# Kernel optimization log

Measured on AMD Instinct MI355X. Metric: run time of the kernel, lower is better.

The kernel has to match this reference:

```python
import jax, jax.numpy as jnp
import numpy as np

B, S, D = 16, 1024, 768          # batch, seq_len, in_features
NS, MAXW = 256, 8                # num_spans, max span width (fixed for jit)
V, C = 128, 6                    # num_vertexes, max corefs per vertex
R = 512                          # num_max_rels_per_example
REL, HID, DIS = 97, 384, 20      # relation_num, hidden_dim, dis_size
NEG = -1e30


def setup_inputs() -> dict:
    key = jax.random.key(0)
    ks = jax.random.split(key, 14)
    sentence_repr = jax.random.normal(ks[0], (B, S, D), jnp.float32)
    starts = jax.random.randint(ks[1], (B, NS), 0, S - MAXW)
    widths = jax.random.randint(ks[2], (B, NS), 0, MAXW)
    entity_span_indices = jnp.stack([starts, starts + widths], axis=-1)  # (B,NS,2), start<=end
    entity_span_indices_mask = jax.random.randint(ks[3], (B, NS), 0, 2)
    vertex_indices = jax.random.randint(ks[4], (B, V, C), 0, NS)
    vertex_indices_mask = jax.random.randint(ks[5], (B, V, C), 0, 2)
    head_tail_indices = jax.random.randint(ks[6], (B, R, 2), 0, V)
    relation_mask = jax.random.randint(ks[7], (B, R), 0, 2)
    dis_h_2_t = jax.random.randint(ks[8], (B, R), 0, 20)
    dis_t_2_h = jax.random.randint(ks[9], (B, R), 0, 20)
    dis_embed = jax.random.normal(ks[10], (20, DIS), jnp.float32) * 0.02
    dis_embed = dis_embed.at[10].set(0.0)  # padding_idx=10
    fin = D + DIS                      # final_in_features with distance
    in_proj = 2 * fin + D              # concat [head+dis, tail+dis, head*tail]
    W1 = jax.random.normal(ks[11], (in_proj, HID), jnp.float32) / np.float32(np.sqrt(in_proj))
    W2 = jax.random.normal(ks[12], (HID, REL), jnp.float32) / np.float32(np.sqrt(HID))
    b2 = jnp.zeros((REL,), jnp.float32)
    return dict(sentence_repr=sentence_repr, entity_span_indices=entity_span_indices,
                entity_span_indices_mask=entity_span_indices_mask,
                vertex_indices=vertex_indices, vertex_indices_mask=vertex_indices_mask,
                head_tail_indices=head_tail_indices, relation_mask=relation_mask,
                dis_h_2_t=dis_h_2_t, dis_t_2_h=dis_t_2_h,
                dis_embed=dis_embed, W1=W1, W2=W2, b2=b2)


def reference(sentence_repr, entity_span_indices, entity_span_indices_mask,
              vertex_indices, vertex_indices_mask, head_tail_indices,
              relation_mask, dis_h_2_t, dis_t_2_h, dis_embed, W1, W2, b2):
    Bx, Sx, Dx = sentence_repr.shape
    # --- SpanExtractor: masked max pooling over tokens in each span [start, end] ---
    starts = entity_span_indices[..., 0]
    ends = entity_span_indices[..., 1]
    pos = starts[..., None] + jnp.arange(MAXW)            # (B,NS,W)
    valid = pos <= ends[..., None]
    posc = jnp.clip(pos, 0, Sx - 1).reshape(Bx, -1)       # (B,NS*W)
    tok = jnp.take_along_axis(sentence_repr, posc[..., None], axis=1)
    tok = tok.reshape(Bx, NS, MAXW, Dx)
    span_emb = jnp.where(valid[..., None], tok, NEG).max(axis=2)   # (B,NS,D)
    # --- coref 'mean' pooling over spans per vertex (batched_index_select) ---
    vidx = vertex_indices.reshape(Bx, -1)
    ve = jnp.take_along_axis(span_emb, vidx[..., None], axis=1).reshape(Bx, V, C, Dx)
    m = vertex_indices_mask.astype(jnp.float32)
    cnt = jnp.maximum(m.sum(axis=2), 1.0)                 # num_corefs clamped >=1
    vertex_emb = (ve * m[..., None]).sum(axis=2) / cnt[..., None]  # (B,V,D)
    # --- head/tail gather ---
    hti = head_tail_indices.reshape(Bx, -1)
    ht = jnp.take_along_axis(vertex_emb, hti[..., None], axis=1).reshape(Bx, R, 2, Dx)
    head_repr = ht[:, :, 0, :]
    tail_repr = ht[:, :, 1, :]
    # (original multiplies by relation_mask and discards the result -> no-op)
    eh = dis_embed[dis_h_2_t]                              # (B,R,DIS)
    et = dis_embed[dis_t_2_h]
    feat = jnp.concatenate([head_repr, eh, tail_repr, et, head_repr * tail_repr], axis=-1)
    # TwoLayerLinear: relu(x @ W1) @ W2 + b2, bias=(False, True)
    predict_re = jax.nn.relu(feat @ W1) @ W2 + b2          # (B,R,REL)
    return predict_re
```

## Files before the change

kernel.cpp:

```cpp
#include <hip/hip_runtime.h>
#include <cstdint>
#include <cstddef>

#define B_    16
#define S_    1024
#define D_    768
#define NS_   256
#define V_    128
#define C_    6
#define R_    512
#define REL_  97
#define HID_  384
#define DIS_  20
#define K1_   2344
#define KP_   2432
#define NIT_  38
#define N2P_  128

#define BM1   128
#define BN1   128
#define SLICE_ ((size_t)8192 * HID_)

typedef unsigned short ushort_t;
typedef unsigned int   u32;
typedef short bf16x4 __attribute__((ext_vector_type(4)));
typedef short bf16x8 __attribute__((ext_vector_type(8)));
typedef float f32x4  __attribute__((ext_vector_type(4)));
typedef float f32x16 __attribute__((ext_vector_type(16)));

__device__ __forceinline__ float bf2f(short s) {
    return __uint_as_float(((unsigned int)(unsigned short)s) << 16);
}
__device__ __forceinline__ short f2bf(float x) {
    union { float f; unsigned int u; } c; c.f = x;
    unsigned int r = (c.u + 0x7fffu + ((c.u >> 16) & 1u)) >> 16;
    return (short)(unsigned short)r;
}

typedef const __attribute__((address_space(1))) u32* gas_t;
typedef __attribute__((address_space(3))) u32*       las_t;
__device__ __forceinline__ void dma16(const void* g, void* l) {
    __builtin_amdgcn_global_load_lds((gas_t)g, (las_t)l, 16, 0, 0);
}

__device__ __forceinline__ int w1_orig(int k) {
    if      (k < 768)  return k;
    else if (k < 1536) return k + 20;
    else if (k < 2304) return k + 40;
    else if (k < 2324) return 768 + (k - 2304);
    else if (k < K1_)  return 1556 + (k - 2324);
    return -1;
}

__global__ __launch_bounds__(192) void prep_kernel(
    const float* __restrict__ sr, const int* __restrict__ spans,
    const float* __restrict__ W1, const float* __restrict__ W2,
    ushort_t* __restrict__ span_emb, ushort_t* __restrict__ W1Tile,
    ushort_t* __restrict__ W2T)
{
    int blk = blockIdx.x;
    int tid = threadIdx.x;
    if (blk < 4096) {
        int bn    = blk;
        int b     = bn >> 8;
        int start = spans[2 * bn];
        int end   = spans[2 * bn + 1];
        int w     = end - start;
        const float* base = sr + ((size_t)b * S_ + start) * D_ + tid * 4;
        f32x4 m = *(const f32x4*)base;
        for (int j = 1; j <= w; ++j) {
            f32x4 x = *(const f32x4*)(base + (size_t)j * D_);
#pragma unroll
            for (int c = 0; c < 4; ++c) m[c] = fmaxf(m[c], x[c]);
        }
        bf16x4 o;
#pragma unroll
        for (int c = 0; c < 4; ++c) o[c] = f2bf(m[c]);
        *(bf16x4*)(span_emb + (size_t)bn * D_ + tid * 4) = o;
    } else if (blk < 4096 + NIT_) {
        int it = blk - 4096;
#pragma unroll
        for (int g = 0; g < 16; ++g) {
            int idx = g * 192 + tid;
            int nn  = idx & 127;
            int kg  = (idx >> 7) & 7;
            int nt  = idx >> 10;
            int n   = nt * 128 + nn;
            bf16x8 p;
#pragma unroll
            for (int j = 0; j < 8; ++j) {
                int k = it * 64 + kg * 8 + j;
                int orig = w1_orig(k);
                float v = (orig >= 0) ? W1[(size_t)orig * HID_ + n] : 0.f;
                p[j] = f2bf(v);
            }
            *(bf16x8*)(W1Tile + (((size_t)it * 3 + nt) * 8 + kg) * 1024 + nn * 8) = p;
        }
    } else {
        int bid = blk - 4096 - NIT_;
#pragma unroll
        for (int i = 0; i < 32; ++i) {
            int e = bid * 6144 + i * 192 + tid;
            int n = e / HID_;
            int k = e - n * HID_;
            float v = (n < REL_) ? W2[(size_t)k * REL_ + n] : 0.f;
            W2T[e] = (ushort_t)f2bf(v);
        }
    }
}

__global__ __launch_bounds__(192) void vertex_kernel(
    const ushort_t* __restrict__ span_emb, const int* __restrict__ vidx,
    const int* __restrict__ vmask, ushort_t* __restrict__ vembB)
{
    int bv = blockIdx.x;
    int b  = bv >> 7;
    const int* vi = vidx  + bv * C_;
    const int* vm = vmask + bv * C_;
    int   idxs[C_];
    float ms[C_];
    float cnt = 0.f;
#pragma unroll
    for (int c = 0; c < C_; ++c) {
        idxs[c] = vi[c];
        ms[c]   = (float)vm[c];
        cnt    += ms[c];
    }
    float inv = 1.f / fmaxf(cnt, 1.f);
    int col = threadIdx.x * 4;
    float s[4] = {0.f, 0.f, 0.f, 0.f};
#pragma unroll
    for (int c = 0; c < C_; ++c) {
        if (ms[c] != 0.f) {
            bf16x4 x = *(const bf16x4*)(span_emb +
                        ((size_t)(b * NS_ + idxs[c])) * D_ + col);
#pragma unroll
            for (int q = 0; q < 4; ++q) s[q] += bf2f(x[q]);
        }
    }
    bf16x4 o;
#pragma unroll
    for (int q = 0; q < 4; ++q) o[q] = f2bf(s[q] * inv);
    *(bf16x4*)(vembB + (size_t)bv * D_ + col) = o;
}

__global__ __launch_bounds__(256, 2) void gemm1_kernel(
    const ushort_t* __restrict__ vembB, const int* __restrict__ ht,
    const int* __restrict__ dht, const int* __restrict__ dth,
    const float* __restrict__ dis, const ushort_t* __restrict__ W1Tile,
    ushort_t* __restrict__ hiddenS)
{
    __shared__ ushort_t Abuf[2][BM1][64];
    __shared__ ushort_t Bbuf[2][8][BN1][8];

    int tid  = threadIdx.x;
    int wv   = tid >> 6;
    int lane = tid & 63;
    int m0   = blockIdx.x * BM1;
    int n0   = blockIdx.y * BN1;
    int nt   = blockIdx.y;
    int ksl  = blockIdx.z;

    int rr  = lane >> 3;
    int sl  = lane & 7;
    int gsw = (sl - rr) & 7;

    int hoff[4], toff[4];
#pragma unroll
    for (int gi = 0; gi < 4; ++gi) {
        int row = wv * 32 + gi * 8 + rr;
        int g   = m0 + row;
        int b   = g >> 9;
        hoff[gi] = (b * V_ + ht[2 * g])     * D_;
        toff[gi] = (b * V_ + ht[2 * g + 1]) * D_;
    }

    auto stage = [&](int bf, int it_g) {
        int k0   = it_g * 64;
        int r    = k0 / 768;
        int koff = k0 - r * 768;
        int kk   = koff + gsw * 8;
        if (r == 0) {
#pragma unroll
            for (int gi = 0; gi < 4; ++gi)
                dma16(vembB + hoff[gi] + kk, &Abuf[bf][wv * 32 + gi * 8][0]);
        } else if (r == 1) {
#pragma unroll
            for (int gi = 0; gi < 4; ++gi)
                dma16(vembB + toff[gi] + kk, &Abuf[bf][wv * 32 + gi * 8][0]);
        } else if (r == 2) {
#pragma unroll
            for (int gi = 0; gi < 4; ++gi) {
                bf16x8 h = *(const bf16x8*)(vembB + hoff[gi] + kk);
                bf16x8 t = *(const bf16x8*)(vembB + toff[gi] + kk);
                bf16x8 p;
#pragma unroll
                for (int j = 0; j < 8; ++j) p[j] = f2bf(bf2f(h[j]) * bf2f(t[j]));
                *(bf16x8*)&Abuf[bf][wv * 32 + gi * 8 + rr][sl * 8] = p;
            }
        } else {
            int kb = k0 - 2304;
#pragma unroll
            for (int gi = 0; gi < 4; ++gi) {
                int g   = m0 + wv * 32 + gi * 8 + rr;
                int rdh = dht[g], rdt = dth[g];
                bf16x8 p;
#pragma unroll
                for (int j = 0; j < 8; ++j) {
                    int kkj = kb + gsw * 8 + j;
                    float v = 0.f;
                    if      (kkj < 20) v = dis[rdh * DIS_ + kkj];
                    else if (kkj < 40) v = dis[rdt * DIS_ + (kkj - 20)];
                    p[j] = f2bf(v);
                }
                *(bf16x8*)&Abuf[bf][wv * 32 + gi * 8 + rr][sl * 8] = p;
            }
        }
        const ushort_t* bbase = W1Tile + ((size_t)it_g * 3 + nt) * 8192;
#pragma unroll
        for (int q = 0; q < 4; ++q) {
            int p = wv * 4 + q;
            dma16(bbase + (size_t)p * 512 + lane * 8,
                  &Bbuf[bf][p >> 1][(p & 1) * 64][0]);
        }
    };

    int half = lane >> 5;
    int lrow = lane & 31;
    int wm   = (wv & 1) * 64;
    int wn   = (wv >> 1) * 64;

    f32x16 acc[2][2];
#pragma unroll
    for (int i = 0; i < 2; ++i)
#pragma unroll
        for (int j = 0; j < 2; ++j)
#pragma unroll
            for (int r = 0; r < 16; ++r) acc[i][j][r] = 0.f;

    stage(0, ksl);
    for (int it = 0; it < 19; ++it) {
        int bf = it & 1;
        __syncthreads();
        if (it + 1 < 19) stage(bf ^ 1, 2 * (it + 1) + ksl);
#pragma unroll
        for (int s = 0; s < 4; ++s) {
            int kg   = s * 2 + half;
            int slot = ((kg + lrow) & 7) * 8;
            bf16x8 a0 = *(bf16x8*)&Abuf[bf][wm + lrow][slot];
            bf16x8 a1 = *(bf16x8*)&Abuf[bf][wm + 32 + lrow][slot];
            bf16x8 b0 = *(bf16x8*)&Bbuf[bf][kg][wn + lrow][0];
            bf16x8 b1 = *(bf16x8*)&Bbuf[bf][kg][wn + 32 + lrow][0];
            acc[0][0] = __builtin_amdgcn_mfma_f32_32x32x16_bf16(a0, b0, acc[0][0], 0, 0, 0);
            acc[0][1] = __builtin_amdgcn_mfma_f32_32x32x16_bf16(a0, b1, acc[0][1], 0, 0, 0);
            acc[1][0] = __builtin_amdgcn_mfma_f32_32x32x16_bf16(a1, b0, acc[1][0], 0, 0, 0);
            acc[1][1] = __builtin_amdgcn_mfma_f32_32x32x16_bf16(a1, b1, acc[1][1], 0, 0, 0);
        }
    }

    ushort_t* outp = hiddenS + (size_t)ksl * SLICE_;
#pragma unroll
    for (int fm = 0; fm < 2; ++fm)
#pragma unroll
        for (int fn = 0; fn < 2; ++fn) {
            int col = n0 + wn + fn * 32 + lrow;
#pragma unroll
            for (int r = 0; r < 16; ++r) {
                int row = m0 + wm + fm * 32 + (r & 3) + 8 * (r >> 2) + 4 * half;
                outp[(size_t)row * HID_ + col] = (ushort_t)f2bf(acc[fm][fn][r]);
            }
        }
}

__global__ __launch_bounds__(256) void gemm2_kernel(
    const ushort_t* __restrict__ hiddenS, const ushort_t* __restrict__ W2T,
    const float* __restrict__ b2, float* __restrict__ out)
{
    __shared__ ushort_t As[32][72];
    __shared__ ushort_t Bs[128][72];

    int m0  = blockIdx.x * 32;
    int tid = threadIdx.x;

    int arow = tid >> 3;
    int akk  = (tid & 7) * 8;

    bf16x8 pA; bf16x8 pB[4];
    auto loadAB = [&](int k0) {
        const ushort_t* hp = hiddenS + (size_t)(m0 + arow) * HID_ + k0 + akk;
        bf16x8 x0 = *(const bf16x8*)hp;
        bf16x8 x1 = *(const bf16x8*)(hp + SLICE_);
#pragma unroll
        for (int j = 0; j < 8; ++j)
            pA[j] = f2bf(fmaxf(bf2f(x0[j]) + bf2f(x1[j]), 0.f));
#pragma unroll
        for (int e = 0; e < 4; ++e)
            pB[e] = *(const bf16x8*)(W2T + (size_t)(arow + e * 32) * HID_ + k0 + akk);
    };

    int w    = tid >> 6;
    int lane = tid & 63;
    int wm = (w & 1) * 16;
    int wn = (w >> 1) * 64;
    int lr = lane & 15, lq = lane >> 4;

    f32x4 acc[4];
#pragma unroll
    for (int e = 0; e < 4; ++e) acc[e] = (f32x4){0.f, 0.f, 0.f, 0.f};

    loadAB(0);
    for (int k0 = 0; k0 < HID_; k0 += 64) {
        __syncthreads();
        *(bf16x8*)&As[arow][akk] = pA;
#pragma unroll
        for (int e = 0; e < 4; ++e)
            *(bf16x8*)&Bs[arow + e * 32][akk] = pB[e];
        __syncthreads();
        if (k0 + 64 < HID_) loadAB(k0 + 64);
#pragma unroll
        for (int ks = 0; ks < 2; ++ks) {
            int kb = ks * 32 + lq * 8;
            bf16x8 a = *(bf16x8*)&As[wm + lr][kb];
#pragma unroll
            for (int nf = 0; nf < 4; ++nf) {
                bf16x8 bb = *(bf16x8*)&Bs[wn + nf * 16 + lr][kb];
                acc[nf] = __builtin_amdgcn_mfma_f32_16x16x32_bf16(a, bb, acc[nf], 0, 0, 0);
            }
        }
    }

    int grow = m0 + wm + lq * 4;
#pragma unroll
    for (int nf = 0; nf < 4; ++nf) {
        int col = wn + nf * 16 + lr;
        if (col < REL_) {
            float bias = b2[col];
#pragma unroll
            for (int r = 0; r < 4; ++r)
                out[(size_t)(grow + r) * REL_ + col] = acc[nf][r] + bias;
        }
    }
}

extern "C" void kernel_launch(void* const* d_in, const int* in_sizes, int n_in,
                              void* d_out, int out_size, void* d_ws, size_t ws_size,
                              hipStream_t stream)
{
    const float* sr    = (const float*)d_in[0];
    const int*   spans = (const int*)  d_in[1];
    const int*   vidx  = (const int*)  d_in[3];
    const int*   vmask = (const int*)  d_in[4];
    const int*   ht    = (const int*)  d_in[5];
    const int*   dht   = (const int*)  d_in[7];
    const int*   dth   = (const int*)  d_in[8];
    const float* dis   = (const float*)d_in[9];
    const float* W1    = (const float*)d_in[10];
    const float* W2    = (const float*)d_in[11];
    const float* b2    = (const float*)d_in[12];
    float* out = (float*)d_out;

    ushort_t* span_emb = (ushort_t*)d_ws;
    ushort_t* vembB    = span_emb + (size_t)B_ * NS_ * D_;
    ushort_t* W1Tile   = vembB + (size_t)B_ * V_ * D_;
    ushort_t* W2T      = W1Tile + (size_t)NIT_ * 3 * 8192;
    ushort_t* hiddenS  = W2T + (size_t)N2P_ * HID_;

    prep_kernel<<<4096 + NIT_ + 8, 192, 0, stream>>>(
        sr, spans, W1, W2, span_emb, W1Tile, W2T);
    vertex_kernel<<<B_ * V_, 192, 0, stream>>>(span_emb, vidx, vmask, vembB);

    dim3 g1((B_ * R_) / BM1, HID_ / BN1, 2);
    gemm1_kernel<<<g1, 256, 0, stream>>>(vembB, ht, dht, dth, dis, W1Tile, hiddenS);

    gemm2_kernel<<<(B_ * R_) / 32, 256, 0, stream>>>(hiddenS, W2T, b2, out);
}
```

Measured before the change: 164.8 us.

## Restructure prep kernel: fixed-width span max loads and wider W1/W2 repack grids

The span max-pool now has each of 256 threads handle three scalar columns and issue all eight row loads up front, masking by width with selects. This removes the data-dependent loop so loads can overlap, at the cost of always reading eight rows. The W1 and W2 repack work is spread over many more blocks (456 and 24 instead of 38 and 8), each thread producing one 16-byte packed chunk. The aim is to stop a few long-running tail blocks from dominating the prep kernel.

```diff
diff --git a/kernel.cpp b/kernel.cpp
--- a/kernel.cpp
+++ b/kernel.cpp
@@ -52,7 +52,7 @@
     return -1;
 }
 
-__global__ __launch_bounds__(192) void prep_kernel(
+__global__ __launch_bounds__(256) void prep_kernel(
     const float* __restrict__ sr, const int* __restrict__ spans,
     const float* __restrict__ W1, const float* __restrict__ W2,
     ushort_t* __restrict__ span_emb, ushort_t* __restrict__ W1Tile,
@@ -66,46 +66,49 @@
         int start = spans[2 * bn];
         int end   = spans[2 * bn + 1];
         int w     = end - start;
-        const float* base = sr + ((size_t)b * S_ + start) * D_ + tid * 4;
-        f32x4 m = *(const f32x4*)base;
-        for (int j = 1; j <= w; ++j) {
-            f32x4 x = *(const f32x4*)(base + (size_t)j * D_);
-#pragma unroll
-            for (int c = 0; c < 4; ++c) m[c] = fmaxf(m[c], x[c]);
-        }
-        bf16x4 o;
-#pragma unroll
-        for (int c = 0; c < 4; ++c) o[c] = f2bf(m[c]);
-        *(bf16x4*)(span_emb + (size_t)bn * D_ + tid * 4) = o;
-    } else if (blk < 4096 + NIT_) {
-        int it = blk - 4096;
-#pragma unroll
-        for (int g = 0; g < 16; ++g) {
-            int idx = g * 192 + tid;
-            int nn  = idx & 127;
-            int kg  = (idx >> 7) & 7;
-            int nt  = idx >> 10;
-            int n   = nt * 128 + nn;
-            bf16x8 p;
-#pragma unroll
-            for (int j = 0; j < 8; ++j) {
-                int k = it * 64 + kg * 8 + j;
-                int orig = w1_orig(k);
-                float v = (orig >= 0) ? W1[(size_t)orig * HID_ + n] : 0.f;
-                p[j] = f2bf(v);
-            }
-            *(bf16x8*)(W1Tile + (((size_t)it * 3 + nt) * 8 + kg) * 1024 + nn * 8) = p;
-        }
+        const float* base = sr + ((size_t)b * S_ + start) * D_;
+        ushort_t* out = span_emb + (size_t)bn * D_;
+#pragma unroll
+        for (int e = 0; e < 3; ++e) {
+            int d = tid + e * 256;
+            float x[8];
+#pragma unroll
+            for (int j = 0; j < 8; ++j)
+                x[j] = base[(size_t)j * D_ + d];
+            float m = x[0];
+#pragma unroll
+            for (int j = 1; j < 8; ++j)
+                m = (j <= w) ? fmaxf(m, x[j]) : m;
+            out[d] = (ushort_t)f2bf(m);
+        }
+    } else if (blk < 4096 + 456) {
+        int flat = (blk - 4096) * 256 + tid;
+        int nn   = flat & 127;
+        int kg   = (flat >> 7) & 7;
+        int itnt = flat >> 10;
+        int nt   = itnt % 3;
+        int it   = itnt / 3;
+        int n    = nt * 128 + nn;
+        bf16x8 p;
+#pragma unroll
+        for (int j = 0; j < 8; ++j) {
+            int k = it * 64 + kg * 8 + j;
+            int orig = w1_orig(k);
+            float v = (orig >= 0) ? W1[(size_t)orig * HID_ + n] : 0.f;
+            p[j] = f2bf(v);
+        }
+        *(bf16x8*)(W1Tile + (((size_t)itnt * 8 + kg) * 1024) + nn * 8) = p;
     } else {
-        int bid = blk - 4096 - NIT_;
-#pragma unroll
-        for (int i = 0; i < 32; ++i) {
-            int e = bid * 6144 + i * 192 + tid;
-            int n = e / HID_;
-            int k = e - n * HID_;
-            float v = (n < REL_) ? W2[(size_t)k * REL_ + n] : 0.f;
-            W2T[e] = (ushort_t)f2bf(v);
-        }
+        int g  = (blk - 4552) * 256 + tid;
+        int n  = g / 48;
+        int k0 = (g - n * 48) * 8;
+        bf16x8 p;
+#pragma unroll
+        for (int j = 0; j < 8; ++j) {
+            float v = (n < REL_) ? W2[(size_t)(k0 + j) * REL_ + n] : 0.f;
+            p[j] = f2bf(v);
+        }
+        *(bf16x8*)(W2T + (size_t)n * HID_ + k0) = p;
     }
 }
 
@@ -365,7 +368,7 @@
     ushort_t* W2T      = W1Tile + (size_t)NIT_ * 3 * 8192;
     ushort_t* hiddenS  = W2T + (size_t)N2P_ * HID_;
 
-    prep_kernel<<<4096 + NIT_ + 8, 192, 0, stream>>>(
+    prep_kernel<<<4096 + 456 + 24, 256, 0, stream>>>(
         sr, spans, W1, W2, span_emb, W1Tile, W2T);
     vertex_kernel<<<B_ * V_, 192, 0, stream>>>(span_emb, vidx, vmask, vembB);
 
```

New measurement: 154.2 us. 6.4% less time.
